# Optimization experiments

Hardware: AMD Instinct MI355X
Metric: run time of the kernel (lower is better)

The kernel has to match this reference:

```python
import jax, jax.numpy as jnp
import numpy as np
from jax import lax

DIM = 128
HEADS = 2
SR = 4
HID = 512  # 4 * DIM
DROPKEY_P = 0.1


def _ln(x, g, b, eps=1e-5):
    m = jnp.mean(x, axis=-1, keepdims=True)
    v = jnp.var(x, axis=-1, keepdims=True)
    return (x - m) / jnp.sqrt(v + eps) * g + b


def _block(x, H, W, params, key):
    (n1g, n1b, qw, kvw, srw, srb, sng, snb, pw, pb,
     n2g, n2b, f1w, f1b, dww, dwb, f2w, f2b) = params
    B, N, C = x.shape
    dh = C // HEADS
    scale = dh ** -0.5
    # --- spatial-reduction attention ---
    h = _ln(x, n1g, n1b)
    q = (h @ qw.T).reshape(B, N, HEADS, dh).transpose(0, 2, 1, 3)  # [B,h,N,dh]
    xi = h.transpose(0, 2, 1).reshape(B, C, H, W)
    xs = lax.conv_general_dilated(xi, srw, (SR, SR), 'VALID',
                                  dimension_numbers=('NCHW', 'OIHW', 'NCHW'))
    xs = xs + srb[None, :, None, None]
    Np = (H // SR) * (W // SR)
    xs = xs.reshape(B, C, Np).transpose(0, 2, 1)  # [B,N',C]
    xs = _ln(xs, sng, snb)
    kv = (xs @ kvw.T).reshape(B, Np, 2, HEADS, dh).transpose(2, 0, 3, 1, 4)
    k, v = kv[0], kv[1]  # [B,h,N',dh]
    attn = jnp.einsum('bhnd,bhmd->bhnm', q, k) * scale
    # dropkey: bernoulli(p) mask pushed to -1e12 before softmax (always applied)
    mask = jax.random.bernoulli(key, DROPKEY_P, attn.shape)
    attn = attn + mask.astype(attn.dtype) * (-1e12)
    attn = jax.nn.softmax(attn, axis=-1)
    o = jnp.einsum('bhnm,bhmd->bhnd', attn, v).transpose(0, 2, 1, 3).reshape(B, N, C)
    x = x + o @ pw.T + pb
    # --- MLP with depthwise conv ---
    h2 = _ln(x, n2g, n2b)
    h2 = h2 @ f1w.T + f1b  # [B,N,HID]
    hi = h2.transpose(0, 2, 1).reshape(B, HID, H, W)
    hi = lax.conv_general_dilated(hi, dww, (1, 1), 'SAME',
                                  feature_group_count=HID,
                                  dimension_numbers=('NCHW', 'OIHW', 'NCHW'))
    hi = hi + dwb[None, :, None, None]
    h2 = hi.reshape(B, HID, N).transpose(0, 2, 1)
    h2 = jax.nn.gelu(h2, approximate=False)
    x = x + h2 @ f2w.T + f2b
    return x


def setup_inputs() -> dict:
    key = jax.random.key(0)
    ks = jax.random.split(key, 10)
    p = {}
    p['x'] = jax.random.normal(ks[0], (16, 2 * DIM, 56, 56), jnp.float32)
    p['concat_w'] = jax.random.normal(ks[1], (DIM, 2 * DIM), jnp.float32) * 0.02
    p['concat_b'] = jnp.zeros((DIM,), jnp.float32)
    # two Blocks -> leading dim 2 on all per-block params
    p['norm1_g'] = jnp.ones((2, DIM), jnp.float32)
    p['norm1_b'] = jnp.zeros((2, DIM), jnp.float32)
    p['q_w'] = jax.random.normal(ks[2], (2, DIM, DIM), jnp.float32) * 0.02
    p['kv_w'] = jax.random.normal(ks[3], (2, 2 * DIM, DIM), jnp.float32) * 0.02
    p['sr_w'] = jax.random.normal(ks[4], (2, DIM, DIM, SR, SR), jnp.float32) * 0.03
    p['sr_b'] = jnp.zeros((2, DIM), jnp.float32)
    p['srn_g'] = jnp.ones((2, DIM), jnp.float32)
    p['srn_b'] = jnp.zeros((2, DIM), jnp.float32)
    p['proj_w'] = jax.random.normal(ks[5], (2, DIM, DIM), jnp.float32) * 0.02
    p['proj_b'] = jnp.zeros((2, DIM), jnp.float32)
    p['norm2_g'] = jnp.ones((2, DIM), jnp.float32)
    p['norm2_b'] = jnp.zeros((2, DIM), jnp.float32)
    p['fc1_w'] = jax.random.normal(ks[6], (2, HID, DIM), jnp.float32) * 0.02
    p['fc1_b'] = jnp.zeros((2, HID), jnp.float32)
    p['dw_w'] = jax.random.normal(ks[7], (2, HID, 1, 3, 3), jnp.float32) * 0.1
    p['dw_b'] = jnp.zeros((2, HID), jnp.float32)
    p['fc2_w'] = jax.random.normal(ks[8], (2, DIM, HID), jnp.float32) * 0.02
    p['fc2_b'] = jnp.zeros((2, DIM), jnp.float32)
    return p


def reference(x, concat_w, concat_b, norm1_g, norm1_b, q_w, kv_w, sr_w, sr_b,
              srn_g, srn_b, proj_w, proj_b, norm2_g, norm2_b, fc1_w, fc1_b,
              dw_w, dw_b, fc2_w, fc2_b):
    b, c, h, w = x.shape
    xs = x.transpose(0, 2, 3, 1).reshape(b, h * w, c)
    xs = xs @ concat_w.T + concat_b  # [B,N,DIM]
    mkey = jax.random.key(42)
    stacked = (norm1_g, norm1_b, q_w, kv_w, sr_w, sr_b, srn_g, srn_b, proj_w,
               proj_b, norm2_g, norm2_b, fc1_w, fc1_b, dw_w, dw_b, fc2_w, fc2_b)
    for i in range(2):
        params_i = tuple(p[i] for p in stacked)
        xs = _block(xs, h, w, params_i, jax.random.fold_in(mkey, i))
    return xs.reshape(b, h, w, DIM).transpose(0, 3, 1, 2)
```

## Files before the change

kernel.cpp:

```cpp
#include <hip/hip_runtime.h>
#include <stdint.h>

typedef __attribute__((ext_vector_type(8))) short short8;
typedef __attribute__((ext_vector_type(4))) float f32x4;
typedef __attribute__((ext_vector_type(2))) float f32x2;
typedef unsigned short u16;
typedef uint32_t u32;
typedef unsigned long long u64;

__host__ __device__ static inline void threefry(u32 k0, u32 k1, u32 x0, u32 x1,
                                                u32* o0, u32* o1) {
  u32 ks2 = k0 ^ k1 ^ 0x1BD11BDAu;
  x0 += k0; x1 += k1;
#define TF_RR(r) { x0 += x1; x1 = (x1 << (r)) | (x1 >> (32 - (r))); x1 ^= x0; }
  TF_RR(13) TF_RR(15) TF_RR(26) TF_RR(6)
  x0 += k1;  x1 += ks2 + 1u;
  TF_RR(17) TF_RR(29) TF_RR(16) TF_RR(24)
  x0 += ks2; x1 += k0 + 2u;
  TF_RR(13) TF_RR(15) TF_RR(26) TF_RR(6)
  x0 += k0;  x1 += k1 + 3u;
  TF_RR(17) TF_RR(29) TF_RR(16) TF_RR(24)
  x0 += k1;  x1 += ks2 + 4u;
  TF_RR(13) TF_RR(15) TF_RR(26) TF_RR(6)
  x0 += ks2; x1 += k0 + 5u;
#undef TF_RR
  *o0 = x0; *o1 = x1;
}

__device__ static inline float bf2f(u16 u) {
  union { u32 i; float f; } v; v.i = ((u32)u) << 16; return v.f;
}
__device__ static inline u16 f2bf(float f) {
  union { float f; u32 i; } v; v.f = f;
  u32 x = v.i;
  return (u16)((x + 0x7FFFu + ((x >> 16) & 1u)) >> 16);
}
__device__ static inline float lo_bf(u32 w) {
  union { u32 i; float f; } v; v.i = w << 16; return v.f;
}
__device__ static inline float hi_bf(u32 w) {
  union { u32 i; float f; } v; v.i = w & 0xFFFF0000u; return v.f;
}
__device__ static inline bool is_f32(const u32* ng) { return ng[0] == 0x3F800000u; }

typedef const uint32_t __attribute__((address_space(1)))* gas_ptr;
typedef uint32_t __attribute__((address_space(3)))* las_ptr;
__device__ static inline void gld16(const u16* g, u16* l) {
  __builtin_amdgcn_global_load_lds((gas_ptr)(const void*)g, (las_ptr)(void*)l, 16, 0, 0);
}

#define MASK_HALF 9834496u

__global__ __launch_bounds__(256) void mask_gen2(u32* __restrict__ MSK2, u32 k0, u32 k1) {
  int t = blockIdx.x * 256 + threadIdx.x;
  if (t >= 351232) return;
  int w = t % 7;
  int rowbh = t / 7;
  u32 base = (u32)rowbh * 196u + (u32)w * 32u;
  int kmax = 196 - w * 32;
  if (kmax > 32) kmax = 32;
  u32 bits0 = 0, bits1 = 0;
  for (int j = 0; j < kmax; j++) {
    u32 o0, o1;
    threefry(k0, k1, base + (u32)j, base + (u32)j + MASK_HALF, &o0, &o1);
    union { u32 u; float f; } u0, u1;
    u0.u = (o0 >> 9) | 0x3F800000u;
    u1.u = (o1 >> 9) | 0x3F800000u;
    if (u0.f - 1.0f < 0.1f) bits0 |= (1u << j);
    if (u1.f - 1.0f < 0.1f) bits1 |= (1u << j);
  }
  MSK2[(size_t)rowbh * 7 + w] = bits0;
  MSK2[(size_t)(rowbh + 50176) * 7 + w] = bits1;
}

struct PtrTab { const void* p[20]; };
#define ARENA_N 963968
#define VT_WORDS 229376

__global__ __launch_bounds__(256) void convert_params(PtrTab tab, u16* __restrict__ arena,
                                                      u32* __restrict__ VT) {
  const int cum[21] = {0, 32768, 32896, 33152, 33408, 66176, 131712, 656000, 656256,
                       656512, 656768, 689536, 689792, 690048, 690304, 821376, 822400,
                       831616, 832640, 963712, 963968};
  int idx = blockIdx.x * 256 + threadIdx.x;
  if (idx >= ARENA_N) {
    int v = idx - ARENA_N;
    if (v < VT_WORDS) VT[v] = 0;
    return;
  }
  bool f32m = (((const u32*)tab.p[2])[0] == 0x3F800000u);
  int t = 0;
  while (idx >= cum[t + 1]) t++;
  int local = idx - cum[t];
  if (t == 16) {
    int blk = local / 4608, r = local - blk * 4608;
    int wi = r >> 9, c = r & 511;
    local = blk * 4608 + c * 9 + wi;
  }
  u16 v;
  if (f32m) v = f2bf(((const float*)tab.p[t])[local]);
  else      v = ((const u16*)tab.p[t])[local];
  arena[idx] = v;
}

__global__ __launch_bounds__(256) void transpose_in(const void* __restrict__ Xin,
                                                    const u32* __restrict__ ng,
                                                    u16* __restrict__ Xt) {
  bool f32m = is_f32(ng);
  __shared__ u16 tile[64][65];
  int n0 = blockIdx.x * 64, c0 = blockIdx.y * 64, b = blockIdx.z;
  int tx = threadIdx.x & 63, ty = threadIdx.x >> 6;
  if (f32m) {
    const float* src = (const float*)Xin + (size_t)b * 256 * 3136;
#pragma unroll
    for (int i = 0; i < 16; i++) {
      int cl = i * 4 + ty;
      tile[cl][tx] = f2bf(src[(size_t)(c0 + cl) * 3136 + n0 + tx]);
    }
  } else {
    const u16* src = (const u16*)Xin + (size_t)b * 256 * 3136;
#pragma unroll
    for (int i = 0; i < 16; i++) {
      int cl = i * 4 + ty;
      tile[cl][tx] = src[(size_t)(c0 + cl) * 3136 + n0 + tx];
    }
  }
  __syncthreads();
  u16* dst = Xt + (size_t)b * 3136 * 256;
#pragma unroll
  for (int i = 0; i < 16; i++) {
    int nl = i * 4 + ty;
    dst[(size_t)(n0 + nl) * 256 + c0 + tx] = tile[tx][nl];
  }
}

__global__ __launch_bounds__(256) void transpose_out(const float* __restrict__ X,
                                                     const u32* __restrict__ ng,
                                                     void* __restrict__ Out) {
  bool f32m = is_f32(ng);
  __shared__ float tile[64][65];
  int n0 = blockIdx.x * 64, d0 = blockIdx.y * 64, b = blockIdx.z;
  int tx = threadIdx.x & 63, ty = threadIdx.x >> 6;
#pragma unroll
  for (int i = 0; i < 16; i++) {
    int nl = i * 4 + ty;
    tile[nl][tx] = X[((size_t)b * 3136 + n0 + nl) * 128 + d0 + tx];
  }
  __syncthreads();
#pragma unroll
  for (int i = 0; i < 16; i++) {
    int dl = i * 4 + ty;
    size_t o = ((size_t)b * 128 + d0 + dl) * 3136 + n0 + tx;
    if (f32m) ((float*)Out)[o] = tile[tx][dl];
    else      ((u16*)Out)[o]   = f2bf(tile[tx][dl]);
  }
}

__global__ __launch_bounds__(256) void im2col_sr(const u16* __restrict__ H,
                                                 u16* __restrict__ Acol) {
  int t = blockIdx.x * 256 + threadIdx.x;
  int c = t & 127;
  int rest = t >> 7;
  int ij = rest & 15;
  int row = rest >> 4;
  int i = ij >> 2, j = ij & 3;
  int bb = row / 196, pp = row - bb * 196;
  int ph = pp / 14, pw = pp - ph * 14;
  int n = (4 * ph + i) * 56 + 4 * pw + j;
  Acol[(size_t)row * 2048 + c * 16 + ij] = H[((size_t)bb * 3136 + n) * 128 + c];
}

__global__ __launch_bounds__(256) __attribute__((amdgpu_waves_per_eu(2, 4)))
void gemm_tiled(const u16* __restrict__ A,
                const u16* __restrict__ W,
                const u16* __restrict__ bias,
                float* __restrict__ outF,
                u16* __restrict__ outB,
                u16* __restrict__ outVT,
                int M, int N, int K, int mode) {
  __shared__ __align__(16) u16 smem[16896];
  u16* AlsP = smem;
  u16* BlsP = smem + 8192;
  int n0 = blockIdx.x * 128, m0 = blockIdx.y * 128;
  int tid = threadIdx.x, wv = tid >> 6, lane = tid & 63;
  int wr = wv >> 1, wc = wv & 1;
  int l15 = lane & 15, hh = lane >> 4, lk = hh * 8;
  int srow = wv * 32 + (lane >> 2);
  int scol = (lane & 3) * 8;

  f32x4 acc[4][4];
#pragma unroll
  for (int m = 0; m < 4; m++)
#pragma unroll
    for (int n = 0; n < 4; n++) acc[m][n] = (f32x4){0.f, 0.f, 0.f, 0.f};

#define STAGE(buf, k0)                                                          \
  {                                                                             \
    _Pragma("unroll") for (int i = 0; i < 2; i++) {                             \
      int ar = m0 + srow + i * 16;                                              \
      if (ar >= M) ar = M - 1;                                                  \
      gld16(A + (size_t)ar * K + (k0) + scol,                                   \
            AlsP + (buf) * 4096 + (wv * 32 + i * 16) * 32);                     \
      int br = n0 + srow + i * 16;                                              \
      gld16(W + (size_t)br * K + (k0) + scol,                                   \
            BlsP + (buf) * 4096 + (wv * 32 + i * 16) * 32);                     \
    }                                                                           \
  }

  int nt = K >> 5;
  STAGE(0, 0);
  int cur = 0;
  for (int t = 0; t < nt; t++) {
    __syncthreads();
    if (t + 1 < nt) STAGE(cur ^ 1, (t + 1) * 32);
    short8 af[4], bf[4];
#pragma unroll
    for (int m = 0; m < 4; m++)
      af[m] = *(const short8*)(AlsP + cur * 4096 + (wr * 64 + m * 16 + l15) * 32 + lk);
#pragma unroll
    for (int n = 0; n < 4; n++)
      bf[n] = *(const short8*)(BlsP + cur * 4096 + (wc * 64 + n * 16 + l15) * 32 + lk);
#pragma unroll
    for (int m = 0; m < 4; m++)
#pragma unroll
      for (int n = 0; n < 4; n++)
        acc[m][n] = __builtin_amdgcn_mfma_f32_16x16x32_bf16(af[m], bf[n], acc[m][n], 0, 0, 0);
    cur ^= 1;
  }
#undef STAGE

  if (mode == 0) {
    __syncthreads();
#pragma unroll
    for (int n = 0; n < 4; n++) {
      int col = wc * 64 + n * 16 + l15;
      float bv = bias ? bf2f(bias[n0 + col]) : 0.0f;
#pragma unroll
      for (int m = 0; m < 4; m++) {
        int rbase = wr * 64 + m * 16 + hh * 4;
#pragma unroll
        for (int r = 0; r < 4; r++)
          smem[(rbase + r) * 132 + col] = f2bf(acc[m][n][r] + bv);
      }
    }
    __syncthreads();
#pragma unroll
    for (int p = 0; p < 8; p++) {
      int row = p * 16 + (tid >> 4);
      int colb = (tid & 15) * 8;
      int grow = m0 + row;
      if (grow < M) {
        short8 v = *(const short8*)&smem[row * 132 + colb];
        *(short8*)(outB + (size_t)grow * N + n0 + colb) = v;
      }
    }
    return;
  }

#pragma unroll
  for (int n = 0; n < 4; n++) {
    int col = n0 + wc * 64 + n * 16 + l15;
    float bv = bias ? bf2f(bias[col]) : 0.0f;
#pragma unroll
    for (int m = 0; m < 4; m++) {
      int rbase = m0 + wr * 64 + m * 16 + hh * 4;
#pragma unroll
      for (int r = 0; r < 4; r++) {
        int row = rbase + r;
        if (row < M) {
          float v = acc[m][n][r] + bv;
          if (mode == 1) outF[(size_t)row * N + col] = v;
          else if (mode == 2) outF[(size_t)row * N + col] += v;
          else {
            if (col < 128) outB[(size_t)row * 128 + col] = f2bf(v);
            else {
              int hd = (col - 128) >> 6, d = (col - 128) & 63;
              int b = row / 196, key = row - b * 196;
              outVT[(size_t)((b * 2 + hd) * 64 + d) * 224 + key] = f2bf(v);
            }
          }
        }
      }
    }
  }
}

__global__ __launch_bounds__(256) __attribute__((amdgpu_waves_per_eu(2, 4)))
void gemm_n128(const u16* __restrict__ A,
               const u16* __restrict__ W,
               const u16* __restrict__ bias,
               float* __restrict__ outF,
               u16* __restrict__ outB,
               const u16* __restrict__ lnG,
               const u16* __restrict__ lnB,
               u16* __restrict__ outH,
               int M, int K, int mode) {
  __shared__ __align__(16) u16 smem[12288];
  __shared__ float sumsA[64][4];
  __shared__ float sumsB[64][4];
  u16* Als = smem;
  u16* Bls = smem + 4096;
  int m0 = blockIdx.y * 64;
  int tid = threadIdx.x, wv = tid >> 6, lane = tid & 63;
  int l15 = lane & 15, hq = lane >> 4, lk = hq * 8;
  int scol = (lane & 3) * 8;

  f32x4 acc[4][2];
#pragma unroll
  for (int m = 0; m < 4; m++)
#pragma unroll
    for (int n = 0; n < 2; n++) acc[m][n] = (f32x4){0.f, 0.f, 0.f, 0.f};

#define STAGE(buf, k0)                                                          \
  {                                                                             \
    int ar = m0 + wv * 16 + (lane >> 2);                                        \
    if (ar >= M) ar = M - 1;                                                    \
    gld16(A + (size_t)ar * K + (k0) + scol, Als + (buf) * 2048 + wv * 512);     \
    _Pragma("unroll") for (int i = 0; i < 2; i++) {                             \
      int br = wv * 32 + i * 16 + (lane >> 2);                                  \
      gld16(W + (size_t)br * K + (k0) + scol,                                   \
            Bls + (buf) * 4096 + wv * 1024 + i * 512);                          \
    }                                                                           \
  }

  int nt = K >> 5;
  STAGE(0, 0);
  int cur = 0;
  for (int t = 0; t < nt; t++) {
    __syncthreads();
    if (t + 1 < nt) STAGE(cur ^ 1, (t + 1) * 32);
    short8 af[4], bf[2];
#pragma unroll
    for (int m = 0; m < 4; m++)
      af[m] = *(const short8*)(Als + cur * 2048 + (m * 16 + l15) * 32 + lk);
#pragma unroll
    for (int n = 0; n < 2; n++)
      bf[n] = *(const short8*)(Bls + cur * 4096 + (wv * 32 + n * 16 + l15) * 32 + lk);
#pragma unroll
    for (int m = 0; m < 4; m++)
#pragma unroll
      for (int n = 0; n < 2; n++)
        acc[m][n] = __builtin_amdgcn_mfma_f32_16x16x32_bf16(af[m], bf[n], acc[m][n], 0, 0, 0);
    cur ^= 1;
  }
#undef STAGE

  if (mode == 2) {
#pragma unroll
    for (int n = 0; n < 2; n++) {
      int col = wv * 32 + n * 16 + l15;
      float bv = bias ? bf2f(bias[col]) : 0.0f;
#pragma unroll
      for (int m = 0; m < 4; m++) {
        int rbase = m0 + m * 16 + hq * 4;
#pragma unroll
        for (int r = 0; r < 4; r++)
          outF[(size_t)(rbase + r) * 128 + col] += acc[m][n][r] + bv;
      }
    }
    return;
  }

  if (mode >= 4) {
#pragma unroll
    for (int n = 0; n < 2; n++) {
      int col = wv * 32 + n * 16 + l15;
      float bv = bias ? bf2f(bias[col]) : 0.0f;
#pragma unroll
      for (int m = 0; m < 4; m++) {
        int rbase = m0 + m * 16 + hq * 4;
#pragma unroll
        for (int r = 0; r < 4; r++) {
          float v = acc[m][n][r] + bv;
          if (mode == 5) v += outF[(size_t)(rbase + r) * 128 + col];
          acc[m][n][r] = v;
          outF[(size_t)(rbase + r) * 128 + col] = v;
        }
      }
    }
#pragma unroll
    for (int m = 0; m < 4; m++) {
#pragma unroll
      for (int r = 0; r < 4; r++) {
        float a = acc[m][0][r] + acc[m][1][r];
        float b = acc[m][0][r] * acc[m][0][r] + acc[m][1][r] * acc[m][1][r];
#pragma unroll
        for (int d = 1; d < 16; d <<= 1) {
          a += __shfl_xor(a, d);
          b += __shfl_xor(b, d);
        }
        if (l15 == 0) {
          int lrow = m * 16 + hq * 4 + r;
          sumsA[lrow][wv] = a;
          sumsB[lrow][wv] = b;
        }
      }
    }
    __syncthreads();
#pragma unroll
    for (int m = 0; m < 4; m++) {
#pragma unroll
      for (int r = 0; r < 4; r++) {
        int lrow = m * 16 + hq * 4 + r;
        float t1 = sumsA[lrow][0] + sumsA[lrow][1] + sumsA[lrow][2] + sumsA[lrow][3];
        float t2 = sumsB[lrow][0] + sumsB[lrow][1] + sumsB[lrow][2] + sumsB[lrow][3];
        float mean = t1 * 0.0078125f;
        float var = t2 * 0.0078125f - mean * mean;
        float inv = 1.0f / sqrtf(var + 1e-5f);
#pragma unroll
        for (int n = 0; n < 2; n++) {
          int col = wv * 32 + n * 16 + l15;
          float g = bf2f(lnG[col]), bb2 = bf2f(lnB[col]);
          smem[lrow * 132 + col] = f2bf((acc[m][n][r] - mean) * inv * g + bb2);
        }
      }
    }
    __syncthreads();
#pragma unroll
    for (int p = 0; p < 4; p++) {
      int row = p * 16 + (tid >> 4);
      int colb = (tid & 15) * 8;
      short8 v = *(const short8*)&smem[row * 132 + colb];
      *(short8*)(outH + (size_t)(m0 + row) * 128 + colb) = v;
    }
    return;
  }

  __syncthreads();
#pragma unroll
  for (int n = 0; n < 2; n++) {
    int col = wv * 32 + n * 16 + l15;
    float bv = bias ? bf2f(bias[col]) : 0.0f;
#pragma unroll
    for (int m = 0; m < 4; m++) {
      int rbase = m * 16 + hq * 4;
#pragma unroll
      for (int r = 0; r < 4; r++)
        smem[(rbase + r) * 132 + col] = f2bf(acc[m][n][r] + bv);
    }
  }
  __syncthreads();
#pragma unroll
  for (int p = 0; p < 4; p++) {
    int row = p * 16 + (tid >> 4);
    int colb = (tid & 15) * 8;
    short8 v = *(const short8*)&smem[row * 132 + colb];
    *(short8*)(outB + (size_t)(m0 + row) * 128 + colb) = v;
  }
}

__global__ __launch_bounds__(256) void gemm_splitk(const u16* __restrict__ A,
                                                   const u16* __restrict__ W,
                                                   float* __restrict__ PS,
                                                   int M, int N, int K) {
  __shared__ __align__(16) u16 Als[2][4096];
  __shared__ __align__(16) u16 Bls[2][4096];
  int n0 = blockIdx.x * 128, m0 = blockIdx.y * 128, ks = blockIdx.z;
  int tid = threadIdx.x, wv = tid >> 6, lane = tid & 63;
  int wr = wv >> 1, wc = wv & 1;
  int l15 = lane & 15, lk = (lane >> 4) * 8;
  int srow = wv * 32 + (lane >> 2);
  int scol = (lane & 3) * 8;

  f32x4 acc[4][4];
#pragma unroll
  for (int m = 0; m < 4; m++)
#pragma unroll
    for (int n = 0; n < 4; n++) acc[m][n] = (f32x4){0.f, 0.f, 0.f, 0.f};

#define STAGE(buf, k0)                                                          \
  {                                                                             \
    _Pragma("unroll") for (int i = 0; i < 2; i++) {                             \
      int ar = m0 + srow + i * 16;                                              \
      if (ar >= M) ar = M - 1;                                                  \
      gld16(A + (size_t)ar * K + (k0) + scol,                                   \
            &Als[buf][(wv * 32 + i * 16) * 32]);                                \
      int br = n0 + srow + i * 16;                                              \
      gld16(W + (size_t)br * K + (k0) + scol,                                   \
            &Bls[buf][(wv * 32 + i * 16) * 32]);                                \
    }                                                                           \
  }

  int kbeg = ks * 128;
  STAGE(0, kbeg);
  int cur = 0;
  for (int t = 0; t < 4; t++) {
    __syncthreads();
    if (t + 1 < 4) STAGE(cur ^ 1, kbeg + (t + 1) * 32);
    short8 af[4], bf[4];
#pragma unroll
    for (int m = 0; m < 4; m++)
      af[m] = *(const short8*)(&Als[cur][(wr * 64 + m * 16 + l15) * 32 + lk]);
#pragma unroll
    for (int n = 0; n < 4; n++)
      bf[n] = *(const short8*)(&Bls[cur][(wc * 64 + n * 16 + l15) * 32 + lk]);
#pragma unroll
    for (int m = 0; m < 4; m++)
#pragma unroll
      for (int n = 0; n < 4; n++)
        acc[m][n] = __builtin_amdgcn_mfma_f32_16x16x32_bf16(af[m], bf[n], acc[m][n], 0, 0, 0);
    cur ^= 1;
  }
#undef STAGE

  float* myPS = PS + (size_t)ks * M * N;
#pragma unroll
  for (int n = 0; n < 4; n++) {
    int col = n0 + wc * 64 + n * 16 + l15;
#pragma unroll
    for (int m = 0; m < 4; m++) {
      int rbase = m0 + wr * 64 + m * 16 + (lane >> 4) * 4;
#pragma unroll
      for (int r = 0; r < 4; r++) {
        int row = rbase + r;
        if (row < M) myPS[(size_t)row * N + col] = acc[m][n][r];
      }
    }
  }
}

__global__ __launch_bounds__(256) void splitk_reduce_ln(const float* __restrict__ PS,
                                                        const u16* __restrict__ bias,
                                                        const u16* __restrict__ G,
                                                        const u16* __restrict__ Bi,
                                                        u16* __restrict__ XSN) {
  __shared__ float red[4][2];
  int tid = threadIdx.x;
  int row = blockIdx.x * 2 + (tid >> 7);
  int col = tid & 127;
  int t = row * 128 + col;
  float s = bf2f(bias[col]);
#pragma unroll
  for (int k = 0; k < 16; k++) s += PS[(size_t)k * 401408 + t];
  float s1 = s, s2 = s * s;
#pragma unroll
  for (int d = 1; d < 64; d <<= 1) {
    s1 += __shfl_xor(s1, d);
    s2 += __shfl_xor(s2, d);
  }
  int wv = tid >> 6;
  if ((tid & 63) == 0) { red[wv][0] = s1; red[wv][1] = s2; }
  __syncthreads();
  int other = wv ^ 1;
  float t1 = red[wv][0] + red[other][0];
  float t2 = red[wv][1] + red[other][1];
  float mean = t1 * 0.0078125f;
  float var = t2 * 0.0078125f - mean * mean;
  float inv = 1.0f / sqrtf(var + 1e-5f);
  XSN[t] = f2bf((s - mean) * inv * bf2f(G[col]) + bf2f(Bi[col]));
}

__global__ __launch_bounds__(256) __attribute__((amdgpu_waves_per_eu(2, 4)))
void attn_kernel(const u16* __restrict__ Q,
                 const u16* __restrict__ Kb,
                 const u16* __restrict__ VT,
                 const u32* __restrict__ M2,
                 u16* __restrict__ O) {
  __shared__ __align__(16) u16 smA[14848];
  int t = blockIdx.x;
  int tp = (t & 7) * 196 + (t >> 3);
  int bh = tp / 49, qt = tp - bh * 49;
  int b = bh >> 1, hd = bh & 1;
  int q0 = qt * 64;
  int tid = threadIdx.x;

  int wv = tid >> 6, lane = tid & 63;
  int l15 = lane & 15, h = lane >> 4, lk = h * 8;

  {
    const u16* ksrc = Kb + (size_t)b * 196 * 128 + hd * 64;
    for (int idx = tid; idx < 1568; idx += 256) {
      int row = idx >> 3, ch = idx & 7;
      short8 v = *(const short8*)(ksrc + (size_t)row * 128 + ch * 8);
      *(short8*)&smA[row * 68 + ch * 8] = v;
    }
  }

  const u16* qp = Q + ((size_t)(b * 3136 + q0 + wv * 16 + l15) * 128) + hd * 64 + lk;
  short8 aq0 = *(const short8*)(qp);
  short8 aq1 = *(const short8*)(qp + 32);
  int rowg = q0 + wv * 16 + h * 4;

  u32 mwv[4][7];
  const u32* mwbase = M2 + (size_t)(bh * 3136 + rowg) * 7;
#pragma unroll
  for (int r = 0; r < 4; r++)
#pragma unroll
    for (int w = 0; w < 7; w++) mwv[r][w] = mwbase[r * 7 + w];

  __syncthreads();

  float sarr[13][4];
#pragma unroll
  for (int cc = 0; cc < 13; cc++) {
    int key = cc * 16 + l15;
    int keyc = key > 195 ? 195 : key;
    short8 kb0 = *(const short8*)&smA[keyc * 68 + lk];
    short8 kb1 = *(const short8*)&smA[keyc * 68 + 32 + lk];
    f32x4 s = {0.f, 0.f, 0.f, 0.f};
    s = __builtin_amdgcn_mfma_f32_16x16x32_bf16(aq0, kb0, s, 0, 0, 0);
    s = __builtin_amdgcn_mfma_f32_16x16x32_bf16(aq1, kb1, s, 0, 0, 0);
#pragma unroll
    for (int r = 0; r < 4; r++) sarr[cc][r] = s[r] * 0.125f;
  }

#pragma unroll
  for (int cc = 0; cc < 13; cc++) {
    bool keyok = (cc * 16 + l15) < 196;
    int pos = (cc & 3) * 16 + l15;
#pragma unroll
    for (int r = 0; r < 4; r++) {
      u64 mm = (cc < 4) ? ((u64)mwv[r][0] | ((u64)mwv[r][1] << 32))
             : (cc < 8) ? ((u64)mwv[r][2] | ((u64)mwv[r][3] << 32))
             : (cc < 12) ? ((u64)mwv[r][4] | ((u64)mwv[r][5] << 32))
                         : ((u64)mwv[r][6]);
      bool drop = (mm >> pos) & 1ull;
      if (!keyok || drop) sarr[cc][r] = -3.0e38f;
    }
  }

  float mx[4] = {sarr[0][0], sarr[0][1], sarr[0][2], sarr[0][3]};
#pragma unroll
  for (int cc = 1; cc < 13; cc++)
#pragma unroll
    for (int r = 0; r < 4; r++) mx[r] = fmaxf(mx[r], sarr[cc][r]);
#pragma unroll
  for (int d = 1; d < 16; d <<= 1)
#pragma unroll
    for (int r = 0; r < 4; r++) mx[r] = fmaxf(mx[r], __shfl_xor(mx[r], d));
  float sm[4] = {0.f, 0.f, 0.f, 0.f};
#pragma unroll
  for (int cc = 0; cc < 13; cc++)
#pragma unroll
    for (int r = 0; r < 4; r++) {
      float p = __expf(sarr[cc][r] - mx[r]);
      sarr[cc][r] = p;
      sm[r] += p;
    }
#pragma unroll
  for (int d = 1; d < 16; d <<= 1)
#pragma unroll
    for (int r = 0; r < 4; r++) sm[r] += __shfl_xor(sm[r], d);
  float inv[4];
#pragma unroll
  for (int r = 0; r < 4; r++)
    asm("v_rcp_f32 %0, %1" : "=v"(inv[r]) : "v"(sm[r]));

  __syncthreads();

#pragma unroll
  for (int cc = 0; cc < 13; cc++)
#pragma unroll
    for (int r = 0; r < 4; r++)
      smA[(wv * 16 + h * 4 + r) * 232 + cc * 16 + l15] = f2bf(sarr[cc][r] * inv[r]);
#pragma unroll
  for (int rj = 0; rj < 4; rj++) smA[(wv * 16 + l15) * 232 + 208 + h * 4 + rj] = 0;

  const u16* vbase = VT + (size_t)(bh * 64) * 224;
  short8 vw[4];
#pragma unroll
  for (int i = 0; i < 4; i++) {
    vw[i] = *(const short8*)(vbase + (size_t)(0 * 16 + l15) * 224 + i * 32 + lk);
  }
#pragma unroll
  for (int dc = 0; dc < 4; dc++) {
    f32x4 oa = {0.f, 0.f, 0.f, 0.f};
#pragma unroll
    for (int kc = 0; kc < 7; kc++) {
      int i = dc * 7 + kc;
      short8 bv = vw[i & 3];
      if (i + 4 < 28) {
        int i2 = i + 4;
        int dc2 = i2 / 7, kc2 = i2 - dc2 * 7;
        vw[i & 3] =
            *(const short8*)(vbase + (size_t)(dc2 * 16 + l15) * 224 + kc2 * 32 + lk);
      }
      short8 a = *(const short8*)&smA[(wv * 16 + l15) * 232 + kc * 32 + lk];
      oa = __builtin_amdgcn_mfma_f32_16x16x32_bf16(a, bv, oa, 0, 0, 0);
    }
#pragma unroll
    for (int r = 0; r < 4; r++) {
      O[((size_t)(b * 3136 + rowg + r) * 128) + hd * 64 + dc * 16 + l15] = f2bf(oa[r]);
    }
  }
}

__global__ __launch_bounds__(256) __attribute__((amdgpu_waves_per_eu(2, 4)))
void dwconv_gelu(const u16* __restrict__ H2,
                 const u16* __restrict__ Wdw,
                 const u16* __restrict__ Bdw,
                 u16* __restrict__ Out) {
  int tid = threadIdx.x;
  int wv = tid >> 6, lane = tid & 63;
  int sb = blockIdx.x;
  int wg = (sb & 7) * 392 + (sb >> 3);
  int strip = wg * 4 + wv;
  int bb = strip / 784;
  int s = strip - bb * 784;
  int y = s / 14, x0 = (s - y * 14) * 4;
  int c0 = lane * 8;

  f32x2 wf[9][4];
#pragma unroll
  for (int t9 = 0; t9 < 9; t9++) {
    short8 w8 = *(const short8*)(Wdw + t9 * 512 + c0);
#pragma unroll
    for (int p = 0; p < 4; p++) {
      u32 w = ((const u32*)&w8)[p];
      wf[t9][p] = (f32x2){lo_bf(w), hi_bf(w)};
    }
  }
  f32x2 acc[4][4];
  {
    short8 b8 = *(const short8*)(Bdw + c0);
#pragma unroll
    for (int p = 0; p < 4; p++) {
      u32 w = ((const u32*)&b8)[p];
      f32x2 bv = {lo_bf(w), hi_bf(w)};
#pragma unroll
      for (int q = 0; q < 4; q++) acc[q][p] = bv;
    }
  }

  const u16* base = H2 + ((size_t)bb * 3136) * 512 + c0;
#pragma unroll
  for (int di = -1; di <= 1; di++) {
    int y2 = y + di;
    if (y2 < 0 || y2 >= 56) continue;
    const u16* rowp = base + (size_t)(y2 * 56) * 512;
#pragma unroll
    for (int j = 0; j < 6; j++) {
      int c = x0 - 1 + j;
      if (c < 0 || c > 55) continue;
      short8 h8 = *(const short8*)(rowp + (size_t)c * 512);
      f32x2 hf[4];
#pragma unroll
      for (int p = 0; p < 4; p++) {
        u32 w = ((const u32*)&h8)[p];
        hf[p] = (f32x2){lo_bf(w), hi_bf(w)};
      }
      int wrow = (di + 1) * 3;
#pragma unroll
      for (int q = 0; q < 4; q++) {
        int dx = j - 1 - q;
        if (dx < -1 || dx > 1) continue;
#pragma unroll
        for (int p = 0; p < 4; p++) acc[q][p] += hf[p] * wf[wrow + dx + 1][p];
      }
    }
  }

  size_t obase = ((size_t)(bb * 3136 + y * 56 + x0)) * 512 + c0;
#pragma unroll
  for (int q = 0; q < 4; q++) {
    short8 ov;
#pragma unroll
    for (int p = 0; p < 4; p++) {
      float g2[2];
#pragma unroll
      for (int e = 0; e < 2; e++) {
        float v = acc[q][p][e];
        float tt = v * v;
        float yn = v * (-2.3022088f - 0.1029434f * tt);
        float ex;
        asm("v_exp_f32 %0, %1" : "=v"(ex) : "v"(yn));
        float den = 1.0f + ex;
        float sg;
        asm("v_rcp_f32 %0, %1" : "=v"(sg) : "v"(den));
        g2[e] = v * sg;
      }
      u32 pk;
      asm("v_cvt_pk_bf16_f32 %0, %1, %2" : "=v"(pk) : "v"(g2[0]), "v"(g2[1]));
      ((u32*)&ov)[p] = pk;
    }
    *(short8*)(Out + obase + (size_t)q * 512) = ov;
  }
}

__global__ __launch_bounds__(256) void fill_sentinel(void* __restrict__ Out,
                                                     const u32* __restrict__ ng, int n) {
  bool f32m = is_f32(ng);
  int t = blockIdx.x * 256 + threadIdx.x;
  if (t >= n) return;
  if (f32m) ((float*)Out)[t] = 12345.0f;
  else      ((u16*)Out)[t]   = f2bf(12345.0f);
}

extern "C" void kernel_launch(void* const* d_in, const int* in_sizes, int n_in,
                              void* d_out, int out_size, void* d_ws, size_t ws_size,
                              hipStream_t stream) {
  (void)in_sizes; (void)n_in;
  const u32* ng = (const u32*)d_in[3];

  const size_t o_X   = 0;
  const size_t o_H   = 25690112;
  const size_t o_R   = o_H + 12845056;
  const size_t o_Q   = o_R;
  const size_t o_O   = o_R + 12845056;
  const size_t o_Xt  = o_R + 25690112;
  const size_t o_H2C = o_R;
  const size_t o_H2  = o_R + 51380224;
  const size_t o_XSN = o_H2 + 51380224;
  const size_t o_KB  = o_XSN + 802816;
  const size_t o_VT  = o_KB + 802816;
  const size_t o_M2  = o_VT + 917504;
  const size_t o_AR  = o_M2 + 2809856;
  const size_t NEED  = o_AR + (size_t)ARENA_N * 2;

  if (ws_size < NEED) {
    fill_sentinel<<<(out_size + 255) / 256, 256, 0, stream>>>(d_out, ng, out_size);
    return;
  }

  char* ws = (char*)d_ws;
  float* X  = (float*)(ws + o_X);
  u16* H    = (u16*)(ws + o_H);
  u16* Qb   = (u16*)(ws + o_Q);
  u16* Ob   = (u16*)(ws + o_O);
  u16* Xt   = (u16*)(ws + o_Xt);
  u16* H2C  = (u16*)(ws + o_H2C);
  u16* H2   = (u16*)(ws + o_H2);
  float* PS = (float*)(ws + o_H2);
  u16* XSN  = (u16*)(ws + o_XSN);
  u16* Kb   = (u16*)(ws + o_KB);
  u16* VT   = (u16*)(ws + o_VT);
  u32* MSK2 = (u32*)(ws + o_M2);
  u16* AR   = (u16*)(ws + o_AR);

  PtrTab tab;
  for (int j = 0; j < 20; j++) tab.p[j] = d_in[j + 1];
  convert_params<<<(ARENA_N + VT_WORDS + 255) / 256, 256, 0, stream>>>(tab, AR, (u32*)VT);

  u16* ACW  = AR + 0;      u16* ACB  = AR + 32768;
  u16* AN1G = AR + 32896;  u16* AN1B = AR + 33152;
  u16* AQW  = AR + 33408;  u16* AKVW = AR + 66176;
  u16* ASRW = AR + 131712; u16* ASRB = AR + 656000;
  u16* ASNG = AR + 656256; u16* ASNB = AR + 656512;
  u16* APW  = AR + 656768; u16* APB  = AR + 689536;
  u16* AN2G = AR + 689792; u16* AN2B = AR + 690048;
  u16* AF1W = AR + 690304; u16* AF1B = AR + 821376;
  u16* ADWW = AR + 822400; u16* ADWB = AR + 831616;
  u16* AF2W = AR + 832640; u16* AF2B = AR + 963712;

  transpose_in<<<dim3(49, 4, 16), 256, 0, stream>>>(d_in[0], ng, Xt);
  gemm_n128<<<dim3(1, 784), 256, 0, stream>>>(Xt, ACW, ACB, X, nullptr,
                                              AN1G, AN1B, H, 50176, 256, 4);

  for (int i = 0; i < 2; i++) {
    u32 fk0, fk1;
    threefry(0u, 42u, 0u, (u32)i, &fk0, &fk1);

    gemm_n128<<<dim3(1, 784), 256, 0, stream>>>(H, AQW + i * 16384, nullptr, nullptr,
                                                Qb, nullptr, nullptr, nullptr,
                                                50176, 128, 0);
    im2col_sr<<<25088, 256, 0, stream>>>(H, Xt);
    gemm_splitk<<<dim3(1, 25, 16), 256, 0, stream>>>(Xt, ASRW + i * 262144, PS,
                                                     3136, 128, 2048);
    mask_gen2<<<1372, 256, 0, stream>>>(MSK2, fk0, fk1);
    splitk_reduce_ln<<<1568, 256, 0, stream>>>(PS, ASRB + i * 128,
                                               ASNG + i * 128, ASNB + i * 128, XSN);

    gemm_tiled<<<dim3(2, 25), 256, 0, stream>>>(XSN, AKVW + i * 32768, nullptr, nullptr,
                                                Kb, VT, 3136, 256, 128, 3);
    attn_kernel<<<1568, 256, 0, stream>>>(Qb, Kb, VT, MSK2, Ob);
    gemm_n128<<<dim3(1, 784), 256, 0, stream>>>(Ob, APW + i * 16384, APB + i * 128,
                                                X, nullptr,
                                                AN2G + i * 128, AN2B + i * 128, H,
                                                50176, 128, 5);
    gemm_tiled<<<dim3(4, 392), 256, 0, stream>>>(H, AF1W + i * 65536, AF1B + i * 512,
                                                 nullptr, H2, nullptr,
                                                 50176, 512, 128, 0);
    dwconv_gelu<<<3136, 256, 0, stream>>>(H2, ADWW + i * 4608, ADWB + i * 512, H2C);
    if (i == 0) {
      gemm_n128<<<dim3(1, 784), 256, 0, stream>>>(H2C, AF2W, AF2B, X, nullptr,
                                                  AN1G + 128, AN1B + 128, H,
                                                  50176, 512, 5);
    } else {
      gemm_n128<<<dim3(1, 784), 256, 0, stream>>>(H2C, AF2W + 65536, AF2B + 128,
                                                  X, nullptr, nullptr, nullptr, nullptr,
                                                  50176, 512, 2);
    }
  }

  transpose_out<<<dim3(49, 2, 16), 256, 0, stream>>>(X, ng, d_out);
}
```

Baseline: 487.4 us.

## Fuse Q projection GEMM into attention kernel

Removes the standalone Q projection launch and computes each head's Q tile inside the attention kernel with MFMA from H and the Q weights. The result is staged through shared memory to reload it in the A-operand layout. This eliminates writing and rereading the Q buffer and one kernel launch. In exchange, H rows are read once per head and the attention kernel does extra MFMA work and register use before the K load.

Measured after the change: 500.0 us. 1.03x slower.

```diff
diff --git a/kernel.cpp b/kernel.cpp
--- a/kernel.cpp
+++ b/kernel.cpp
@@ -551,7 +551,8 @@
 }
 
 __global__ __launch_bounds__(256) __attribute__((amdgpu_waves_per_eu(2, 4)))
-void attn_kernel(const u16* __restrict__ Q,
+void attn_kernel(const u16* __restrict__ H,
+                 const u16* __restrict__ Wq,
                  const u16* __restrict__ Kb,
                  const u16* __restrict__ VT,
                  const u32* __restrict__ M2,
@@ -566,6 +567,40 @@
 
   int wv = tid >> 6, lane = tid & 63;
   int l15 = lane & 15, h = lane >> 4, lk = h * 8;
+  int rowg = q0 + wv * 16 + h * 4;
+
+  {
+    f32x4 qacc[4];
+#pragma unroll
+    for (int n = 0; n < 4; n++) qacc[n] = (f32x4){0.f, 0.f, 0.f, 0.f};
+    const u16* hrow = H + (size_t)(b * 3136 + q0 + wv * 16 + l15) * 128 + lk;
+#pragma unroll
+    for (int kc = 0; kc < 4; kc++) {
+      short8 ah = *(const short8*)(hrow + kc * 32);
+#pragma unroll
+      for (int n = 0; n < 4; n++) {
+        short8 bw = *(const short8*)(Wq + (size_t)(hd * 64 + n * 16 + l15) * 128 +
+                                     kc * 32 + lk);
+        qacc[n] = __builtin_amdgcn_mfma_f32_16x16x32_bf16(ah, bw, qacc[n], 0, 0, 0);
+      }
+    }
+#pragma unroll
+    for (int n = 0; n < 4; n++)
+#pragma unroll
+      for (int r = 0; r < 4; r++)
+        smA[(wv * 16 + h * 4 + r) * 68 + n * 16 + l15] = f2bf(qacc[n][r]);
+  }
+  short8 aq0 = *(const short8*)&smA[(wv * 16 + l15) * 68 + lk];
+  short8 aq1 = *(const short8*)&smA[(wv * 16 + l15) * 68 + 32 + lk];
+
+  u32 mwv[4][7];
+  const u32* mwbase = M2 + (size_t)(bh * 3136 + rowg) * 7;
+#pragma unroll
+  for (int r = 0; r < 4; r++)
+#pragma unroll
+    for (int w = 0; w < 7; w++) mwv[r][w] = mwbase[r * 7 + w];
+
+  __syncthreads();
 
   {
     const u16* ksrc = Kb + (size_t)b * 196 * 128 + hd * 64;
@@ -575,19 +610,6 @@
       *(short8*)&smA[row * 68 + ch * 8] = v;
     }
   }
-
-  const u16* qp = Q + ((size_t)(b * 3136 + q0 + wv * 16 + l15) * 128) + hd * 64 + lk;
-  short8 aq0 = *(const short8*)(qp);
-  short8 aq1 = *(const short8*)(qp + 32);
-  int rowg = q0 + wv * 16 + h * 4;
-
-  u32 mwv[4][7];
-  const u32* mwbase = M2 + (size_t)(bh * 3136 + rowg) * 7;
-#pragma unroll
-  for (int r = 0; r < 4; r++)
-#pragma unroll
-    for (int w = 0; w < 7; w++) mwv[r][w] = mwbase[r * 7 + w];
-
   __syncthreads();
 
   float sarr[13][4];
@@ -806,6 +828,7 @@
   const size_t o_M2  = o_VT + 917504;
   const size_t o_AR  = o_M2 + 2809856;
   const size_t NEED  = o_AR + (size_t)ARENA_N * 2;
+  (void)o_Q;
 
   if (ws_size < NEED) {
     fill_sentinel<<<(out_size + 255) / 256, 256, 0, stream>>>(d_out, ng, out_size);
@@ -815,7 +838,6 @@
   char* ws = (char*)d_ws;
   float* X  = (float*)(ws + o_X);
   u16* H    = (u16*)(ws + o_H);
-  u16* Qb   = (u16*)(ws + o_Q);
   u16* Ob   = (u16*)(ws + o_O);
   u16* Xt   = (u16*)(ws + o_Xt);
   u16* H2C  = (u16*)(ws + o_H2C);
@@ -850,9 +872,6 @@
     u32 fk0, fk1;
     threefry(0u, 42u, 0u, (u32)i, &fk0, &fk1);
 
-    gemm_n128<<<dim3(1, 784), 256, 0, stream>>>(H, AQW + i * 16384, nullptr, nullptr,
-                                                Qb, nullptr, nullptr, nullptr,
-                                                50176, 128, 0);
     im2col_sr<<<25088, 256, 0, stream>>>(H, Xt);
     gemm_splitk<<<dim3(1, 25, 16), 256, 0, stream>>>(Xt, ASRW + i * 262144, PS,
                                                      3136, 128, 2048);
@@ -862,7 +881,7 @@
 
     gemm_tiled<<<dim3(2, 25), 256, 0, stream>>>(XSN, AKVW + i * 32768, nullptr, nullptr,
                                                 Kb, VT, 3136, 256, 128, 3);
-    attn_kernel<<<1568, 256, 0, stream>>>(Qb, Kb, VT, MSK2, Ob);
+    attn_kernel<<<1568, 256, 0, stream>>>(H, AQW + i * 16384, Kb, VT, MSK2, Ob);
     gemm_n128<<<dim3(1, 784), 256, 0, stream>>>(Ob, APW + i * 16384, APB + i * 128,
                                                 X, nullptr,
                                                 AN2G + i * 128, AN2B + i * 128, H,
```
